# Kernel tuning notes

Hardware: AMD Instinct MI355X
Metric: run time of the kernel (lower is better)

The kernel has to match this reference:

```python
import jax, jax.numpy as jnp
import numpy as np

N_NODES = 50000
N_EDGES = 1600000
IN_DIM = 256
OUT_DIM = 128
T = 8
V_THRESHOLD = 1.0
TAU = 2.0
STEP_SIZE = 0.1


def setup_inputs() -> dict:
    key = jax.random.key(0)
    k1, k2, k3 = jax.random.split(key, 3)
    x = jax.random.normal(k1, (N_NODES, IN_DIM), dtype=jnp.float32)
    W = jax.random.normal(k2, (IN_DIM, OUT_DIM), dtype=jnp.float32) / np.sqrt(IN_DIM)
    edge_index = jax.random.randint(k3, (2, N_EDGES), 0, N_NODES, dtype=jnp.int64)
    return {"x": x, "W": W, "edge_index": edge_index}


def gcn_conv(x, W, edge_index):
    # GCNConv (no bias): h = D^{-1/2} (A + I) D^{-1/2} (x @ W)
    n = x.shape[0]
    h = x @ W  # [N, OUT]
    loops = jnp.arange(n, dtype=edge_index.dtype)
    src = jnp.concatenate([edge_index[0], loops])
    dst = jnp.concatenate([edge_index[1], loops])
    deg = jax.ops.segment_sum(jnp.ones_like(dst, dtype=h.dtype), dst, num_segments=n)
    dinv = jnp.where(deg > 0, jax.lax.rsqrt(deg), 0.0)
    norm = dinv[src] * dinv[dst]  # [E+N]
    msgs = h[src] * norm[:, None]
    return jax.ops.segment_sum(msgs, dst, num_segments=n)  # [N, OUT]


def reference(x, W, edge_index):
    h = gcn_conv(x, W, edge_index)            # encoder output, [N, OUT]
    u = h * STEP_SIZE                          # per-step tangent input
    z0 = jnp.zeros_like(h)                     # manifold origin

    def step(z, _):
        # leaky charge toward input current, fire on threshold, soft reset
        Hm = z + (u - z) / TAU
        o = (Hm >= V_THRESHOLD).astype(Hm.dtype)
        z_new = Hm - o * V_THRESHOLD
        return z_new, (o, z_new)

    _, (o_seq, z_seq) = jax.lax.scan(step, z0, None, length=T)
    return o_seq, z_seq  # each [T, N, OUT]
```

## Files before the change

kernel.cpp:

```cpp
#include <hip/hip_runtime.h>
#include <hip/hip_bf16.h>

#define N_NODES 50000
#define N_EDGES 1600000
#define IN_DIM  256
#define OUT_DIM 128
#define T_STEPS 8

typedef __attribute__((ext_vector_type(8))) short bf16x8;
typedef __attribute__((ext_vector_type(4))) float f32x4;


__device__ inline unsigned short bf_hi_trunc(float x) {
    return (unsigned short)(__float_as_uint(x) >> 16);
}
__device__ inline float bf_to_f(unsigned short u) {
    return __uint_as_float((unsigned)u << 16);
}
__device__ inline unsigned short f2bf_rne(float a) {
    __hip_bfloat16 t = __float2bfloat16(a);
    return *(unsigned short*)&t;
}
__device__ inline float bf_lo(unsigned p) { return __uint_as_float(p << 16); }
__device__ inline float bf_hi(unsigned p) { return __uint_as_float(p & 0xffff0000u); }
__device__ inline unsigned pack2(float a, float b) {
    return (unsigned)f2bf_rne(a) | ((unsigned)f2bf_rne(b) << 16);
}

__global__ void k_prep_w(const float* __restrict__ W,
                         unsigned short* __restrict__ Wt_hi,
                         unsigned short* __restrict__ Wt_lo) {
    int idx = blockIdx.x * 256 + threadIdx.x;
    int n = idx >> 8;
    int k = idx & 255;
    float w = W[k * OUT_DIM + n];
    unsigned short hi = bf_hi_trunc(w);
    Wt_hi[idx] = hi;
    Wt_lo[idx] = f2bf_rne(w - bf_to_f(hi));
}

__global__ __launch_bounds__(256) void
k_gemm_count(const float* __restrict__ x,
             const unsigned short* __restrict__ Wt_hi,
             const unsigned short* __restrict__ Wt_lo,
             float* __restrict__ h,
             const int* __restrict__ edge, int* __restrict__ cnt) {
    int tg = blockIdx.x * 256 + threadIdx.x;
    for (int e = tg; e < N_EDGES; e += 782 * 256)
        atomicAdd(&cnt[edge[N_EDGES + e]], 1);

    int wave = blockIdx.x * 4 + (threadIdx.x >> 6);
    if (wave >= N_NODES / 16) return;
    int lane = threadIdx.x & 63;
    int quad = lane >> 4;
    int r16  = lane & 15;
    int m0 = wave * 16;

    f32x4 acc[8];
#pragma unroll
    for (int nt = 0; nt < 8; ++nt) acc[nt] = (f32x4){0.f, 0.f, 0.f, 0.f};

#pragma unroll
    for (int kt = 0; kt < 8; ++kt) {
        int k0 = kt * 32 + quad * 8;
        const float* xp = x + (size_t)(m0 + r16) * IN_DIM + k0;
        float4 v0 = *(const float4*)xp;
        float4 v1 = *(const float4*)(xp + 4);
        float vv[8] = {v0.x, v0.y, v0.z, v0.w, v1.x, v1.y, v1.z, v1.w};
        union { bf16x8 v; unsigned short u[8]; } ahi, alo;
#pragma unroll
        for (int j = 0; j < 8; ++j) {
            unsigned short hi = bf_hi_trunc(vv[j]);
            ahi.u[j] = hi;
            alo.u[j] = f2bf_rne(vv[j] - bf_to_f(hi));
        }
#pragma unroll
        for (int nt = 0; nt < 8; ++nt) {
            size_t woff = (size_t)(nt * 16 + r16) * IN_DIM + k0;
            bf16x8 bhi = *(const bf16x8*)(Wt_hi + woff);
            bf16x8 blo = *(const bf16x8*)(Wt_lo + woff);
            acc[nt] = __builtin_amdgcn_mfma_f32_16x16x32_bf16(ahi.v, bhi, acc[nt], 0, 0, 0);
            acc[nt] = __builtin_amdgcn_mfma_f32_16x16x32_bf16(alo.v, bhi, acc[nt], 0, 0, 0);
            acc[nt] = __builtin_amdgcn_mfma_f32_16x16x32_bf16(ahi.v, blo, acc[nt], 0, 0, 0);
        }
    }
#pragma unroll
    for (int nt = 0; nt < 8; ++nt) {
#pragma unroll
        for (int r = 0; r < 4; ++r) {
            int row = m0 + quad * 4 + r;
            int col = nt * 16 + r16;
            h[(size_t)row * OUT_DIM + col] = acc[nt][r];
        }
    }
}

__global__ __launch_bounds__(1024) void
k_scan(const int* __restrict__ cnt, int* __restrict__ offs,
       float* __restrict__ dinv) {
    __shared__ int sdata[1024];
    const int ITEMS = (N_NODES + 1023) / 1024;
    int tid = threadIdx.x;
    int start = tid * ITEMS;
    int end = min(start + ITEMS, N_NODES);
    int sum = 0;
    for (int i = start; i < end; ++i) sum += cnt[i];
    sdata[tid] = sum;
    __syncthreads();
    for (int off = 1; off < 1024; off <<= 1) {
        int t = (tid >= off) ? sdata[tid - off] : 0;
        __syncthreads();
        sdata[tid] += t;
        __syncthreads();
    }
    int run = sdata[tid] - sum;
    for (int i = start; i < end; ++i) {
        int v = cnt[i];
        offs[i] = run;
        dinv[i] = rsqrtf((float)(v + 1));
        run += v;
    }
}

__global__ void k_scale(const float* __restrict__ h, const float* __restrict__ dinv,
                        unsigned* __restrict__ hs) {
    int idx = blockIdx.x * 256 + threadIdx.x;
    int node = idx >> 6;
    float di = dinv[node];
    float2 hv = ((const float2*)h)[idx];
    hs[idx] = pack2(hv.x * di, hv.y * di);
}

__global__ void k_fill(const int* __restrict__ edge, const int* __restrict__ offs,
                       int* __restrict__ fill, int* __restrict__ csr) {
    int e = blockIdx.x * 256 + threadIdx.x;
    if (e < N_EDGES) {
        int dst = edge[N_EDGES + e];
        int src = edge[e];
        int pos = offs[dst] + atomicAdd(&fill[dst], 1);
        csr[pos] = src;
    }
}

__global__ __launch_bounds__(256) void
k_agg_snn(const unsigned* __restrict__ hs,
          const int* __restrict__ offs, const int* __restrict__ cnt,
          const float* __restrict__ dinv, const int* __restrict__ csr,
          float* __restrict__ out) {
    int node = blockIdx.x * 4 + (threadIdx.x >> 6);
    int lane = threadIdx.x & 63;

    unsigned p = hs[node * 64 + lane];
    float a0 = bf_lo(p), a1 = bf_hi(p);

    int beg = offs[node];
    int end = beg + cnt[node];
    int j = beg;
    for (; j + 8 <= end; j += 8) {
        int s0 = csr[j+0], s1 = csr[j+1], s2 = csr[j+2], s3 = csr[j+3];
        int s4 = csr[j+4], s5 = csr[j+5], s6 = csr[j+6], s7 = csr[j+7];
        unsigned q0 = hs[s0*64+lane], q1 = hs[s1*64+lane];
        unsigned q2 = hs[s2*64+lane], q3 = hs[s3*64+lane];
        unsigned q4 = hs[s4*64+lane], q5 = hs[s5*64+lane];
        unsigned q6 = hs[s6*64+lane], q7 = hs[s7*64+lane];
        a0 += bf_lo(q0); a1 += bf_hi(q0);
        a0 += bf_lo(q1); a1 += bf_hi(q1);
        a0 += bf_lo(q2); a1 += bf_hi(q2);
        a0 += bf_lo(q3); a1 += bf_hi(q3);
        a0 += bf_lo(q4); a1 += bf_hi(q4);
        a0 += bf_lo(q5); a1 += bf_hi(q5);
        a0 += bf_lo(q6); a1 += bf_hi(q6);
        a0 += bf_lo(q7); a1 += bf_hi(q7);
    }
    for (; j < end; ++j) {
        int s = csr[j];
        unsigned q = hs[s*64+lane];
        a0 += bf_lo(q); a1 += bf_hi(q);
    }

    float di = dinv[node];
    float u0 = a0 * di * 0.1f, u1 = a1 * di * 0.1f;
    float z0 = 0.f, z1 = 0.f;
    float2* out2 = (float2*)out;
    size_t baseo = (size_t)node * 64 + lane;
    const size_t plane = (size_t)N_NODES * 64;
#pragma unroll
    for (int t = 0; t < T_STEPS; ++t) {
        float H0 = z0 + (u0 - z0) * 0.5f;
        float H1 = z1 + (u1 - z1) * 0.5f;
        float o0 = (H0 >= 1.0f) ? 1.0f : 0.0f;
        float o1 = (H1 >= 1.0f) ? 1.0f : 0.0f;
        z0 = H0 - o0;
        z1 = H1 - o1;
        out2[(size_t)t * plane + baseo] = make_float2(o0, o1);
        out2[(size_t)(T_STEPS + t) * plane + baseo] = make_float2(z0, z1);
    }
}

extern "C" void kernel_launch(void* const* d_in, const int* in_sizes, int n_in,
                              void* d_out, int out_size, void* d_ws, size_t ws_size,
                              hipStream_t stream) {
    const float* x  = (const float*)d_in[0];
    const float* W  = (const float*)d_in[1];
    const int*   ei = (const int*)d_in[2];
    float* out = (float*)d_out;

    char* ws = (char*)d_ws;
    float*          h     = (float*)(ws + 0);
    unsigned*       hs    = (unsigned*)(ws + 25600000);
    unsigned short* Wt_hi = (unsigned short*)(ws + 38400000);
    unsigned short* Wt_lo = (unsigned short*)(ws + 38465536);
    int*            cnt   = (int*)(ws + 38531072);
    int*            fill  = (int*)(ws + 38731072);
    int*            offs  = (int*)(ws + 38931072);
    float*          dinv  = (float*)(ws + 39131072);
    int*            csr   = (int*)(ws + 39331072);

    hipMemsetAsync(ws + 38531072, 0, 400000, stream);

    k_prep_w<<<128, 256, 0, stream>>>(W, Wt_hi, Wt_lo);
    k_gemm_count<<<782, 256, 0, stream>>>(x, Wt_hi, Wt_lo, h, ei, cnt);
    k_scan<<<1, 1024, 0, stream>>>(cnt, offs, dinv);
    k_scale<<<12500, 256, 0, stream>>>(h, dinv, hs);
    k_fill<<<6250, 256, 0, stream>>>(ei, offs, fill, csr);
    k_agg_snn<<<12500, 256, 0, stream>>>(hs, offs, cnt, dinv, csr, out);
}
```

Before: 789.4 us.

## Restructure pipeline: parallel scan, fuse dinv scaling into GEMM, vectorize CSR build

The single-block serial scan is replaced by a three-kernel multi-block scan that also seeds the fill array with offsets. The GEMM is decoupled from degree counting and now scales by dinv and writes bf16 directly, which removes the fp32 h buffer and the separate scale kernel. Degree counting and CSR fill read edges as int4 with fewer threads, and the aggregation uses wave-uniform bounds and nontemporal output stores. The trade is more kernel launches and a GEMM that now has to wait for the scan to finish.

```diff
diff --git a/kernel.cpp b/kernel.cpp
--- a/kernel.cpp
+++ b/kernel.cpp
@@ -23,32 +23,99 @@
 }
 __device__ inline float bf_lo(unsigned p) { return __uint_as_float(p << 16); }
 __device__ inline float bf_hi(unsigned p) { return __uint_as_float(p & 0xffff0000u); }
-__device__ inline unsigned pack2(float a, float b) {
-    return (unsigned)f2bf_rne(a) | ((unsigned)f2bf_rne(b) << 16);
-}
-
-__global__ void k_prep_w(const float* __restrict__ W,
-                         unsigned short* __restrict__ Wt_hi,
-                         unsigned short* __restrict__ Wt_lo) {
+
+__global__ __launch_bounds__(256) void
+k_prep_count(const float* __restrict__ W,
+             unsigned short* __restrict__ Wt_hi,
+             unsigned short* __restrict__ Wt_lo,
+             const int* __restrict__ edge, int* __restrict__ cnt) {
     int idx = blockIdx.x * 256 + threadIdx.x;
-    int n = idx >> 8;
-    int k = idx & 255;
-    float w = W[k * OUT_DIM + n];
-    unsigned short hi = bf_hi_trunc(w);
-    Wt_hi[idx] = hi;
-    Wt_lo[idx] = f2bf_rne(w - bf_to_f(hi));
-}
-
-__global__ __launch_bounds__(256) void
-k_gemm_count(const float* __restrict__ x,
-             const unsigned short* __restrict__ Wt_hi,
-             const unsigned short* __restrict__ Wt_lo,
-             float* __restrict__ h,
-             const int* __restrict__ edge, int* __restrict__ cnt) {
-    int tg = blockIdx.x * 256 + threadIdx.x;
-    for (int e = tg; e < N_EDGES; e += 782 * 256)
-        atomicAdd(&cnt[edge[N_EDGES + e]], 1);
-
+    const int4* dst4 = (const int4*)(edge + N_EDGES);
+    for (int e = idx; e < N_EDGES / 4; e += 800 * 256) {
+        int4 d = dst4[e];
+        atomicAdd(&cnt[d.x], 1);
+        atomicAdd(&cnt[d.y], 1);
+        atomicAdd(&cnt[d.z], 1);
+        atomicAdd(&cnt[d.w], 1);
+    }
+    if (idx < 32768) {
+        int n = idx >> 8;
+        int k = idx & 255;
+        float w = W[k * OUT_DIM + n];
+        unsigned short hi = bf_hi_trunc(w);
+        Wt_hi[idx] = hi;
+        Wt_lo[idx] = f2bf_rne(w - bf_to_f(hi));
+    }
+}
+
+__global__ __launch_bounds__(256) void
+k_scanA(const int* __restrict__ cnt, int* __restrict__ part) {
+    int t = threadIdx.x;
+    int i4 = blockIdx.x * 256 + t;
+    int4 v = make_int4(0, 0, 0, 0);
+    if (i4 < 12500) v = ((const int4*)cnt)[i4];
+    int s = v.x + v.y + v.z + v.w;
+    __shared__ int sd[256];
+    sd[t] = s; __syncthreads();
+    for (int o = 128; o > 0; o >>= 1) {
+        if (t < o) sd[t] += sd[t + o];
+        __syncthreads();
+    }
+    if (t == 0) part[blockIdx.x] = sd[0];
+}
+
+__global__ void k_scanB(int* __restrict__ part) {
+    int l = threadIdx.x;
+    int v = (l < 49) ? part[l] : 0;
+    int orig = v;
+    for (int o = 1; o < 64; o <<= 1) {
+        int u = __shfl_up(v, o);
+        if (l >= o) v += u;
+    }
+    if (l < 49) part[l] = v - orig;
+}
+
+__global__ __launch_bounds__(256) void
+k_scanC(const int* __restrict__ cnt, const int* __restrict__ part,
+        int* __restrict__ offs, int* __restrict__ fill,
+        float* __restrict__ dinv) {
+    int t = threadIdx.x;
+    int i4 = blockIdx.x * 256 + t;
+    int4 v = make_int4(0, 0, 0, 0);
+    if (i4 < 12500) v = ((const int4*)cnt)[i4];
+    int s = v.x + v.y + v.z + v.w;
+    __shared__ int sd[256];
+    sd[t] = s; __syncthreads();
+    for (int o = 1; o < 256; o <<= 1) {
+        int u = (t >= o) ? sd[t - o] : 0;
+        __syncthreads();
+        sd[t] += u;
+        __syncthreads();
+    }
+    if (i4 < 12500) {
+        int base = part[blockIdx.x] + sd[t] - s;
+        int4 o4;
+        o4.x = base;
+        o4.y = o4.x + v.x;
+        o4.z = o4.y + v.y;
+        o4.w = o4.z + v.z;
+        ((int4*)offs)[i4] = o4;
+        ((int4*)fill)[i4] = o4;
+        float4 d4;
+        d4.x = rsqrtf((float)(v.x + 1));
+        d4.y = rsqrtf((float)(v.y + 1));
+        d4.z = rsqrtf((float)(v.z + 1));
+        d4.w = rsqrtf((float)(v.w + 1));
+        ((float4*)dinv)[i4] = d4;
+    }
+}
+
+__global__ __launch_bounds__(256) void
+k_gemm(const float* __restrict__ x,
+       const unsigned short* __restrict__ Wt_hi,
+       const unsigned short* __restrict__ Wt_lo,
+       const float* __restrict__ dinv,
+       unsigned short* __restrict__ hs) {
     int wave = blockIdx.x * 4 + (threadIdx.x >> 6);
     if (wave >= N_NODES / 16) return;
     int lane = threadIdx.x & 63;
@@ -84,61 +151,32 @@
             acc[nt] = __builtin_amdgcn_mfma_f32_16x16x32_bf16(ahi.v, blo, acc[nt], 0, 0, 0);
         }
     }
+    float dr[4];
+#pragma unroll
+    for (int r = 0; r < 4; ++r) dr[r] = dinv[m0 + quad * 4 + r];
 #pragma unroll
     for (int nt = 0; nt < 8; ++nt) {
 #pragma unroll
         for (int r = 0; r < 4; ++r) {
             int row = m0 + quad * 4 + r;
             int col = nt * 16 + r16;
-            h[(size_t)row * OUT_DIM + col] = acc[nt][r];
+            hs[(size_t)row * OUT_DIM + col] = f2bf_rne(acc[nt][r] * dr[r]);
         }
     }
 }
 
-__global__ __launch_bounds__(1024) void
-k_scan(const int* __restrict__ cnt, int* __restrict__ offs,
-       float* __restrict__ dinv) {
-    __shared__ int sdata[1024];
-    const int ITEMS = (N_NODES + 1023) / 1024;
-    int tid = threadIdx.x;
-    int start = tid * ITEMS;
-    int end = min(start + ITEMS, N_NODES);
-    int sum = 0;
-    for (int i = start; i < end; ++i) sum += cnt[i];
-    sdata[tid] = sum;
-    __syncthreads();
-    for (int off = 1; off < 1024; off <<= 1) {
-        int t = (tid >= off) ? sdata[tid - off] : 0;
-        __syncthreads();
-        sdata[tid] += t;
-        __syncthreads();
-    }
-    int run = sdata[tid] - sum;
-    for (int i = start; i < end; ++i) {
-        int v = cnt[i];
-        offs[i] = run;
-        dinv[i] = rsqrtf((float)(v + 1));
-        run += v;
-    }
-}
-
-__global__ void k_scale(const float* __restrict__ h, const float* __restrict__ dinv,
-                        unsigned* __restrict__ hs) {
-    int idx = blockIdx.x * 256 + threadIdx.x;
-    int node = idx >> 6;
-    float di = dinv[node];
-    float2 hv = ((const float2*)h)[idx];
-    hs[idx] = pack2(hv.x * di, hv.y * di);
-}
-
-__global__ void k_fill(const int* __restrict__ edge, const int* __restrict__ offs,
-                       int* __restrict__ fill, int* __restrict__ csr) {
-    int e = blockIdx.x * 256 + threadIdx.x;
-    if (e < N_EDGES) {
-        int dst = edge[N_EDGES + e];
-        int src = edge[e];
-        int pos = offs[dst] + atomicAdd(&fill[dst], 1);
-        csr[pos] = src;
+__global__ __launch_bounds__(256) void
+k_fill(const int* __restrict__ edge, int* __restrict__ fill,
+       int* __restrict__ csr) {
+    int e4 = blockIdx.x * 256 + threadIdx.x;
+    if (e4 < N_EDGES / 4) {
+        int4 s = ((const int4*)edge)[e4];
+        int4 d = ((const int4*)(edge + N_EDGES))[e4];
+        int p;
+        p = atomicAdd(&fill[d.x], 1); csr[p] = s.x;
+        p = atomicAdd(&fill[d.y], 1); csr[p] = s.y;
+        p = atomicAdd(&fill[d.z], 1); csr[p] = s.z;
+        p = atomicAdd(&fill[d.w], 1); csr[p] = s.w;
     }
 }
 
@@ -153,8 +191,8 @@
     unsigned p = hs[node * 64 + lane];
     float a0 = bf_lo(p), a1 = bf_hi(p);
 
-    int beg = offs[node];
-    int end = beg + cnt[node];
+    int beg = __builtin_amdgcn_readfirstlane(offs[node]);
+    int end = __builtin_amdgcn_readfirstlane(offs[node] + cnt[node]);
     int j = beg;
     for (; j + 8 <= end; j += 8) {
         int s0 = csr[j+0], s1 = csr[j+1], s2 = csr[j+2], s3 = csr[j+3];
@@ -184,6 +222,7 @@
     float2* out2 = (float2*)out;
     size_t baseo = (size_t)node * 64 + lane;
     const size_t plane = (size_t)N_NODES * 64;
+    union F2U { float2 f; unsigned long long u; };
 #pragma unroll
     for (int t = 0; t < T_STEPS; ++t) {
         float H0 = z0 + (u0 - z0) * 0.5f;
@@ -192,8 +231,13 @@
         float o1 = (H1 >= 1.0f) ? 1.0f : 0.0f;
         z0 = H0 - o0;
         z1 = H1 - o1;
-        out2[(size_t)t * plane + baseo] = make_float2(o0, o1);
-        out2[(size_t)(T_STEPS + t) * plane + baseo] = make_float2(z0, z1);
+        F2U a, b;
+        a.f = make_float2(o0, o1);
+        b.f = make_float2(z0, z1);
+        __builtin_nontemporal_store(a.u,
+            (unsigned long long*)(out2 + (size_t)t * plane + baseo));
+        __builtin_nontemporal_store(b.u,
+            (unsigned long long*)(out2 + (size_t)(T_STEPS + t) * plane + baseo));
     }
 }
 
@@ -206,22 +250,23 @@
     float* out = (float*)d_out;
 
     char* ws = (char*)d_ws;
-    float*          h     = (float*)(ws + 0);
-    unsigned*       hs    = (unsigned*)(ws + 25600000);
-    unsigned short* Wt_hi = (unsigned short*)(ws + 38400000);
-    unsigned short* Wt_lo = (unsigned short*)(ws + 38465536);
-    int*            cnt   = (int*)(ws + 38531072);
-    int*            fill  = (int*)(ws + 38731072);
-    int*            offs  = (int*)(ws + 38931072);
-    float*          dinv  = (float*)(ws + 39131072);
-    int*            csr   = (int*)(ws + 39331072);
-
-    hipMemsetAsync(ws + 38531072, 0, 400000, stream);
-
-    k_prep_w<<<128, 256, 0, stream>>>(W, Wt_hi, Wt_lo);
-    k_gemm_count<<<782, 256, 0, stream>>>(x, Wt_hi, Wt_lo, h, ei, cnt);
-    k_scan<<<1, 1024, 0, stream>>>(cnt, offs, dinv);
-    k_scale<<<12500, 256, 0, stream>>>(h, dinv, hs);
-    k_fill<<<6250, 256, 0, stream>>>(ei, offs, fill, csr);
-    k_agg_snn<<<12500, 256, 0, stream>>>(hs, offs, cnt, dinv, csr, out);
-}
+    unsigned short* hs    = (unsigned short*)(ws + 0);
+    unsigned short* Wt_hi = (unsigned short*)(ws + 12800000);
+    unsigned short* Wt_lo = (unsigned short*)(ws + 12865536);
+    int*            cnt   = (int*)(ws + 12931072);
+    int*            fill  = (int*)(ws + 13131072);
+    int*            offs  = (int*)(ws + 13331072);
+    float*          dinv  = (float*)(ws + 13531072);
+    int*            part  = (int*)(ws + 13731072);
+    int*            csr   = (int*)(ws + 13731328);
+
+    hipMemsetAsync(cnt, 0, 200000, stream);
+
+    k_prep_count<<<800, 256, 0, stream>>>(W, Wt_hi, Wt_lo, ei, cnt);
+    k_scanA<<<49, 256, 0, stream>>>(cnt, part);
+    k_scanB<<<1, 64, 0, stream>>>(part);
+    k_scanC<<<49, 256, 0, stream>>>(cnt, part, offs, fill, dinv);
+    k_gemm<<<782, 256, 0, stream>>>(x, Wt_hi, Wt_lo, dinv, hs);
+    k_fill<<<1563, 256, 0, stream>>>(ei, fill, csr);
+    k_agg_snn<<<12500, 256, 0, stream>>>((const unsigned*)hs, offs, cnt, dinv, csr, out);
+}
```

New measurement: 709.3 us. 1.11x faster.
